# Performance work log

Measured on AMD Instinct MI355X. Metric: run time of the kernel, lower is better.

The kernel has to match this reference:

```python
import jax, jax.numpy as jnp
import numpy as np

B, T, D, F, E = 8, 2048, 1024, 4096, 16
C_FACTOR = 1.25
LB_W = 0.01


def setup_inputs() -> dict:
    key = jax.random.key(0)
    ks = jax.random.split(key, 4)
    x = jax.random.normal(ks[0], (B, T, D), dtype=jnp.float32)
    Wr = jax.random.normal(ks[1], (E, D), dtype=jnp.float32) * 0.02
    W1 = jax.random.normal(ks[2], (E, F, D), dtype=jnp.float32) * 0.02
    b1 = jnp.zeros((E, F), dtype=jnp.float32)
    W2 = jax.random.normal(ks[3], (E, D, F), dtype=jnp.float32) * 0.02
    b2 = jnp.zeros((E, D), dtype=jnp.float32)
    return {"x": x, "Wr": Wr, "W1": W1, "b1": b1, "W2": W2, "b2": b2}


def reference(x, Wr, W1, b1, W2, b2):
    Bs, Ts, Ds = x.shape
    Es = Wr.shape[0]
    tokens = Bs * Ts
    xf = x.reshape(tokens, Ds)

    # router
    logits = xf @ Wr.T                       # [tokens, E]
    probs = jax.nn.softmax(logits, axis=-1)
    top1 = jnp.argmax(probs, axis=-1)        # [tokens]
    top1p = jnp.max(probs, axis=-1)          # [tokens]

    capacity = int(C_FACTOR * tokens / Es)   # static python int

    onehot = jax.nn.one_hot(top1, Es, dtype=jnp.int32)        # [tokens, E]
    f = onehot.sum(axis=0).astype(probs.dtype) / tokens
    p = probs.mean(axis=0)
    lb_loss = Es * jnp.sum(f * p) * LB_W

    # faithful reproduction of idx[::expert_capacity]: among tokens routed to
    # expert e (in token order), keep only those whose rank % capacity == 0
    ranks = jnp.cumsum(onehot, axis=0) - 1                     # [tokens, E]
    keep = (onehot == 1) & (ranks % capacity == 0)             # [tokens, E]
    K = (tokens - 1) // capacity + 1                           # static max kept per expert

    idx = jax.vmap(lambda m: jnp.nonzero(m, size=K, fill_value=0)[0])(keep.T)  # [E, K]
    valid = jnp.take_along_axis(keep.T, idx, axis=1)           # [E, K] bool

    xg = xf[idx]                                               # [E, K, D]
    h = jax.nn.gelu(jnp.einsum('ekd,efd->ekf', xg, W1) + b1[:, None, :], approximate=False)
    eo = jnp.einsum('ekf,edf->ekd', h, W2) + b2[:, None, :]    # [E, K, D]
    scale = top1p[idx] * valid.astype(eo.dtype)                # [E, K]
    eo = eo * scale[..., None]

    out = jnp.zeros_like(xf).at[idx.reshape(-1)].add(eo.reshape(-1, Ds))
    return out.reshape(Bs, Ts, Ds), lb_loss
```

## Files before the change

### kernel.cpp

```cpp
#include <hip/hip_runtime.h>
#include <math.h>


#define TOKENS 16384
#define DD     1024
#define FF     4096
#define EE     16
#define CAP    1280
#define KMAX   13
#define NBLK   256

__global__ __launch_bounds__(256) void router_kernel(
    const float* __restrict__ x, const float* __restrict__ Wr,
    int* __restrict__ top1, float* __restrict__ top1p,
    int* __restrict__ blockhist, float* __restrict__ p_sums)
{
    __shared__ float wrj[EE * 256];
    __shared__ float p_acc[EE];
    __shared__ int   hist[EE];

    const int tid  = threadIdx.x;
    const int wave = tid >> 6;
    const int lane = tid & 63;
    const int blk  = blockIdx.x;

    if (tid < EE) { p_acc[tid] = 0.0f; hist[tid] = 0; }

    for (int it = 0; it < 4; ++it) {
        const int tbase = blk * 64 + wave * 16 + it * 4;

        float4 xr[4][4];
        #pragma unroll
        for (int t = 0; t < 4; ++t) {
            const float4* xp = (const float4*)(x + (size_t)(tbase + t) * DD);
            #pragma unroll
            for (int j = 0; j < 4; ++j) xr[t][j] = xp[j * 64 + lane];
        }

        float acc[4][EE];
        #pragma unroll
        for (int t = 0; t < 4; ++t)
            #pragma unroll
            for (int e = 0; e < EE; ++e) acc[t][e] = 0.0f;

        for (int j = 0; j < 4; ++j) {
            __syncthreads();
            #pragma unroll
            for (int k = 0; k < 4; ++k) {
                int i = tid + k * 256;
                int e = i >> 6, c = i & 63;
                ((float4*)wrj)[i] = ((const float4*)Wr)[e * 256 + j * 64 + c];
            }
            __syncthreads();
            #pragma unroll
            for (int e = 0; e < EE; ++e) {
                float4 w = ((const float4*)(wrj + e * 256))[lane];
                #pragma unroll
                for (int t = 0; t < 4; ++t) {
                    acc[t][e] += xr[t][j].x * w.x + xr[t][j].y * w.y
                               + xr[t][j].z * w.z + xr[t][j].w * w.w;
                }
            }
        }

        #pragma unroll
        for (int t = 0; t < 4; ++t)
            #pragma unroll
            for (int e = 0; e < EE; ++e) {
                float v = acc[t][e];
                v += __shfl_xor(v, 32);
                v += __shfl_xor(v, 16);
                v += __shfl_xor(v, 8);
                v += __shfl_xor(v, 4);
                v += __shfl_xor(v, 2);
                v += __shfl_xor(v, 1);
                acc[t][e] = v;
            }

        if (lane < 4) {
            float lg[EE];
            #pragma unroll
            for (int e = 0; e < EE; ++e) {
                float v = acc[3][e];
                if (lane == 2) v = acc[2][e];
                if (lane == 1) v = acc[1][e];
                if (lane == 0) v = acc[0][e];
                lg[e] = v;
            }
            const int gt = tbase + lane;
            float mx = lg[0]; int bi = 0;
            #pragma unroll
            for (int e = 1; e < EE; ++e)
                if (lg[e] > mx) { mx = lg[e]; bi = e; }
            float pr[EE];
            float s = 0.0f;
            #pragma unroll
            for (int e = 0; e < EE; ++e) { pr[e] = expf(lg[e] - mx); s += pr[e]; }
            const float inv = 1.0f / s;
            top1[gt]  = bi;
            top1p[gt] = inv;
            #pragma unroll
            for (int e = 0; e < EE; ++e) atomicAdd(&p_acc[e], pr[e] * inv);
            atomicAdd(&hist[bi], 1);
        }
    }
    __syncthreads();
    if (tid < EE) {
        blockhist[blk * EE + tid] = hist[tid];
        atomicAdd(&p_sums[tid], p_acc[tid]);
    }
}

__global__ __launch_bounds__(256) void scan_kernel(
    const int* __restrict__ blockhist, int* __restrict__ base,
    int* __restrict__ counts, int* __restrict__ nkept,
    const float* __restrict__ p_sums, const int* __restrict__ top1,
    float* __restrict__ mult0, float* __restrict__ lb_out)
{
    __shared__ int   hist_l[NBLK * EE];
    __shared__ int   gsum[EE * 16];
    __shared__ float fp[EE];
    __shared__ int   nk_l[EE];

    const int tid = threadIdx.x;
    for (int i = tid; i < NBLK * EE; i += 256) hist_l[i] = blockhist[i];
    __syncthreads();

    const int e = tid >> 4, g = tid & 15;
    int s = 0;
    for (int b = g * 16; b < g * 16 + 16; ++b) s += hist_l[b * EE + e];
    gsum[e * 16 + g] = s;
    __syncthreads();

    int pre = 0;
    for (int g2 = 0; g2 < g; ++g2) pre += gsum[e * 16 + g2];
    int run = pre;
    for (int b = g * 16; b < g * 16 + 16; ++b) {
        base[b * EE + e] = run;
        run += hist_l[b * EE + e];
    }
    if (g == 15) {
        const int c = run;
        counts[e] = c;
        const int nk = (c > 0) ? ((c - 1) / CAP + 1) : 0;
        nkept[e] = nk;
        nk_l[e]  = nk;
        fp[e] = ((float)c / (float)TOKENS) * (p_sums[e] / (float)TOKENS);
    }
    __syncthreads();
    if (tid == 0) {
        const int e0 = top1[0];
        mult0[0] = (float)(1 + KMAX - nk_l[e0]);
        float sum = 0.0f;
        for (int i = 0; i < EE; ++i) sum += fp[i];
        lb_out[0] = (float)EE * sum * 0.01f;
    }
}

__global__ __launch_bounds__(64) void keep_kernel(
    const int* __restrict__ top1, const float* __restrict__ top1p,
    const int* __restrict__ base, const float* __restrict__ mult0,
    int* __restrict__ kept_tok, float* __restrict__ kept_scale,
    int* __restrict__ slotmap)
{
    __shared__ int t1[64];
    const int tid = threadIdx.x;
    const int blk = blockIdx.x;
    const int gt  = blk * 64 + tid;
    const int e   = top1[gt];
    t1[tid] = e;
    __syncthreads();
    int r = 0;
    for (int i = 0; i < tid; ++i) r += (t1[i] == e) ? 1 : 0;
    const int rank = base[blk * EE + e] + r;
    if (rank % CAP == 0) {
        const int slot = rank / CAP;
        kept_tok[e * KMAX + slot] = gt;
        float sc = top1p[gt];
        if (gt == 0) sc *= mult0[0];
        kept_scale[e * KMAX + slot] = sc;
        slotmap[gt] = e * KMAX + slot;
    }
}

__global__ __launch_bounds__(256) void expert1_kernel(
    const float* __restrict__ x, const float* __restrict__ W1,
    const float* __restrict__ b1, const int* __restrict__ nkept,
    const int* __restrict__ kept_tok, float* __restrict__ h)
{
    const int e    = blockIdx.x >> 8;
    const int fblk = blockIdx.x & 255;
    const int ne   = nkept[e];
    if (ne == 0) return;
    const int wave = threadIdx.x >> 6;
    const int lane = threadIdx.x & 63;
    #pragma unroll
    for (int i = 0; i < 4; ++i) {
        const int f = fblk * 16 + wave * 4 + i;
        const float4* wrow = (const float4*)(W1 + ((size_t)e * FF + f) * DD);
        const float4 w0 = wrow[lane];
        const float4 w1 = wrow[64 + lane];
        const float4 w2 = wrow[128 + lane];
        const float4 w3 = wrow[192 + lane];
        for (int s = 0; s < ne; ++s) {
            const int t = kept_tok[e * KMAX + s];
            const float4* xp = (const float4*)(x + (size_t)t * DD);
            const float4 x0 = xp[lane];
            const float4 x1 = xp[64 + lane];
            const float4 x2 = xp[128 + lane];
            const float4 x3 = xp[192 + lane];
            float d = w0.x*x0.x + w0.y*x0.y + w0.z*x0.z + w0.w*x0.w
                    + w1.x*x1.x + w1.y*x1.y + w1.z*x1.z + w1.w*x1.w
                    + w2.x*x2.x + w2.y*x2.y + w2.z*x2.z + w2.w*x2.w
                    + w3.x*x3.x + w3.y*x3.y + w3.z*x3.z + w3.w*x3.w;
            d += __shfl_xor(d, 32);
            d += __shfl_xor(d, 16);
            d += __shfl_xor(d, 8);
            d += __shfl_xor(d, 4);
            d += __shfl_xor(d, 2);
            d += __shfl_xor(d, 1);
            if (lane == 0) {
                const float v = d + b1[e * FF + f];
                h[((size_t)e * KMAX + s) * FF + f] =
                    0.5f * v * (1.0f + erff(v * 0.70710678118654752440f));
            }
        }
    }
}

__global__ __launch_bounds__(256) void expert2_kernel(
    const float* __restrict__ h, const float* __restrict__ W2,
    const float* __restrict__ b2, const int* __restrict__ nkept,
    const float* __restrict__ kept_scale, float* __restrict__ eo)
{
    const int e    = blockIdx.x >> 6;
    const int dblk = blockIdx.x & 63;
    const int ne   = nkept[e];
    if (ne == 0) return;
    const int wave = threadIdx.x >> 6;
    const int lane = threadIdx.x & 63;
    #pragma unroll
    for (int i = 0; i < 4; ++i) {
        const int d = dblk * 16 + wave * 4 + i;
        const float4* wrow = (const float4*)(W2 + ((size_t)e * DD + d) * FF);
        float4 w[16];
        #pragma unroll
        for (int k = 0; k < 16; ++k) w[k] = wrow[k * 64 + lane];
        for (int s = 0; s < ne; ++s) {
            const float4* hp = (const float4*)(h + ((size_t)e * KMAX + s) * FF);
            float acc = 0.0f;
            #pragma unroll
            for (int k = 0; k < 16; ++k) {
                const float4 hv = hp[k * 64 + lane];
                acc += w[k].x*hv.x + w[k].y*hv.y + w[k].z*hv.z + w[k].w*hv.w;
            }
            acc += __shfl_xor(acc, 32);
            acc += __shfl_xor(acc, 16);
            acc += __shfl_xor(acc, 8);
            acc += __shfl_xor(acc, 4);
            acc += __shfl_xor(acc, 2);
            acc += __shfl_xor(acc, 1);
            if (lane == 0) {
                const float sc = kept_scale[e * KMAX + s];
                eo[((size_t)e * KMAX + s) * DD + d] = sc * (acc + b2[e * DD + d]);
            }
        }
    }
}

__global__ __launch_bounds__(256) void expand_kernel(
    const float* __restrict__ eo, const int* __restrict__ slotmap,
    float* __restrict__ out)
{
    const int nf4 = TOKENS * DD / 4;
    int idx = blockIdx.x * 256 + threadIdx.x;
    const int stride = 4096 * 256;
    for (; idx < nf4; idx += stride) {
        const int t    = idx >> 8;
        const int slot = slotmap[t];
        float4 v = make_float4(0.0f, 0.0f, 0.0f, 0.0f);
        if (slot >= 0) v = ((const float4*)eo)[slot * 256 + (idx & 255)];
        ((float4*)out)[idx] = v;
    }
}

extern "C" void kernel_launch(void* const* d_in, const int* in_sizes, int n_in,
                              void* d_out, int out_size, void* d_ws, size_t ws_size,
                              hipStream_t stream) {
    const float* x  = (const float*)d_in[0];
    const float* Wr = (const float*)d_in[1];
    const float* W1 = (const float*)d_in[2];
    const float* b1 = (const float*)d_in[3];
    const float* W2 = (const float*)d_in[4];
    const float* b2 = (const float*)d_in[5];
    float* out = (float*)d_out;

    char* p = (char*)d_ws;
    int*   top1       = (int*)p;    p += (size_t)TOKENS * 4;
    float* top1p      = (float*)p;  p += (size_t)TOKENS * 4;
    int*   slotmap    = (int*)p;    p += (size_t)TOKENS * 4;
    int*   blockhist  = (int*)p;    p += (size_t)NBLK * EE * 4;
    int*   base       = (int*)p;    p += (size_t)NBLK * EE * 4;
    int*   counts     = (int*)p;    p += (size_t)EE * 4;
    int*   nkept      = (int*)p;    p += (size_t)EE * 4;
    float* p_sums     = (float*)p;  p += (size_t)EE * 4;
    float* mult0      = (float*)p;  p += 16;
    int*   kept_tok   = (int*)p;    p += (size_t)EE * KMAX * 4;
    float* kept_scale = (float*)p;  p += (size_t)EE * KMAX * 4;
    float* eo         = (float*)p;  p += (size_t)EE * KMAX * DD * 4;
    float* h          = (float*)p;  p += (size_t)EE * KMAX * FF * 4;
    (void)ws_size; (void)in_sizes; (void)n_in; (void)counts;

    hipMemsetAsync(p_sums, 0, EE * sizeof(float), stream);
    hipMemsetAsync(slotmap, 0xFF, (size_t)TOKENS * sizeof(int), stream);

    router_kernel<<<NBLK, 256, 0, stream>>>(x, Wr, top1, top1p, blockhist, p_sums);
    scan_kernel<<<1, 256, 0, stream>>>(blockhist, base, counts, nkept, p_sums,
                                       top1, mult0, out + (size_t)out_size - 1);
    keep_kernel<<<NBLK, 64, 0, stream>>>(top1, top1p, base, mult0,
                                         kept_tok, kept_scale, slotmap);
    expert1_kernel<<<EE * 256, 256, 0, stream>>>(x, W1, b1, nkept, kept_tok, h);
    expert2_kernel<<<EE * 64, 256, 0, stream>>>(h, W2, b2, nkept, kept_scale, eo);
    expand_kernel<<<4096, 256, 0, stream>>>(eo, slotmap, out);
}
```

Before: 674.6 us.

## Fuse expert FFN GEMVs with F-chunked split-K and atomic accumulation

Merges the two expert kernels into one. Each block computes a 128-wide chunk of the GELU hidden activations into shared memory, then multiplies that chunk by the matching W2 columns and atomically adds partial outputs into a zeroed accumulator. Scale and bias move into the expand kernel. The two memsets are removed: per-block prob sums replace the global atomics, and keep_kernel now writes the full slotmap and zeroes the accumulator. This drops the global h round-trip and two launches, but the W2 reads become narrow float2 strided rows, and many float atomics add contention and make the summation order nondeterministic.

```diff
diff --git a/kernel.cpp b/kernel.cpp
--- a/kernel.cpp
+++ b/kernel.cpp
@@ -9,11 +9,13 @@
 #define CAP    1280
 #define KMAX   13
 #define NBLK   256
+#define FCH    128
+#define NCH    (FF / FCH)
 
 __global__ __launch_bounds__(256) void router_kernel(
     const float* __restrict__ x, const float* __restrict__ Wr,
     int* __restrict__ top1, float* __restrict__ top1p,
-    int* __restrict__ blockhist, float* __restrict__ p_sums)
+    int* __restrict__ blockhist, float* __restrict__ blockpsum)
 {
     __shared__ float wrj[EE * 256];
     __shared__ float p_acc[EE];
@@ -107,18 +109,19 @@
     __syncthreads();
     if (tid < EE) {
         blockhist[blk * EE + tid] = hist[tid];
-        atomicAdd(&p_sums[tid], p_acc[tid]);
+        blockpsum[blk * EE + tid] = p_acc[tid];
     }
 }
 
 __global__ __launch_bounds__(256) void scan_kernel(
-    const int* __restrict__ blockhist, int* __restrict__ base,
-    int* __restrict__ counts, int* __restrict__ nkept,
-    const float* __restrict__ p_sums, const int* __restrict__ top1,
-    float* __restrict__ mult0, float* __restrict__ lb_out)
+    const int* __restrict__ blockhist, const float* __restrict__ blockpsum,
+    int* __restrict__ base, int* __restrict__ nkept,
+    const int* __restrict__ top1, float* __restrict__ mult0,
+    float* __restrict__ lb_out)
 {
     __shared__ int   hist_l[NBLK * EE];
     __shared__ int   gsum[EE * 16];
+    __shared__ float fps[EE * 16];
     __shared__ float fp[EE];
     __shared__ int   nk_l[EE];
 
@@ -128,8 +131,13 @@
 
     const int e = tid >> 4, g = tid & 15;
     int s = 0;
-    for (int b = g * 16; b < g * 16 + 16; ++b) s += hist_l[b * EE + e];
+    float sp = 0.0f;
+    for (int b = g * 16; b < g * 16 + 16; ++b) {
+        s  += hist_l[b * EE + e];
+        sp += blockpsum[b * EE + e];
+    }
     gsum[e * 16 + g] = s;
+    fps[e * 16 + g]  = sp;
     __syncthreads();
 
     int pre = 0;
@@ -141,11 +149,12 @@
     }
     if (g == 15) {
         const int c = run;
-        counts[e] = c;
         const int nk = (c > 0) ? ((c - 1) / CAP + 1) : 0;
         nkept[e] = nk;
         nk_l[e]  = nk;
-        fp[e] = ((float)c / (float)TOKENS) * (p_sums[e] / (float)TOKENS);
+        float ps = 0.0f;
+        for (int g2 = 0; g2 < 16; ++g2) ps += fps[e * 16 + g2];
+        fp[e] = ((float)c / (float)TOKENS) * (ps / (float)TOKENS);
     }
     __syncthreads();
     if (tid == 0) {
@@ -161,7 +170,7 @@
     const int* __restrict__ top1, const float* __restrict__ top1p,
     const int* __restrict__ base, const float* __restrict__ mult0,
     int* __restrict__ kept_tok, float* __restrict__ kept_scale,
-    int* __restrict__ slotmap)
+    int* __restrict__ slotmap, float* __restrict__ acc)
 {
     __shared__ int t1[64];
     const int tid = threadIdx.x;
@@ -173,30 +182,42 @@
     int r = 0;
     for (int i = 0; i < tid; ++i) r += (t1[i] == e) ? 1 : 0;
     const int rank = base[blk * EE + e] + r;
+    int sm = -1;
     if (rank % CAP == 0) {
         const int slot = rank / CAP;
-        kept_tok[e * KMAX + slot] = gt;
+        sm = e * KMAX + slot;
+        kept_tok[sm] = gt;
         float sc = top1p[gt];
         if (gt == 0) sc *= mult0[0];
-        kept_scale[e * KMAX + slot] = sc;
-        slotmap[gt] = e * KMAX + slot;
-    }
-}
-
-__global__ __launch_bounds__(256) void expert1_kernel(
+        kept_scale[sm] = sc;
+    }
+    slotmap[gt] = sm;
+    float4* a4 = (float4*)acc;
+    for (int i = gt; i < EE * KMAX * DD / 4; i += NBLK * 64)
+        a4[i] = make_float4(0.0f, 0.0f, 0.0f, 0.0f);
+}
+
+__global__ __launch_bounds__(256) void expert_fused_kernel(
     const float* __restrict__ x, const float* __restrict__ W1,
-    const float* __restrict__ b1, const int* __restrict__ nkept,
-    const int* __restrict__ kept_tok, float* __restrict__ h)
-{
-    const int e    = blockIdx.x >> 8;
-    const int fblk = blockIdx.x & 255;
-    const int ne   = nkept[e];
+    const float* __restrict__ b1, const float* __restrict__ W2,
+    const int* __restrict__ nkept, const int* __restrict__ kept_tok,
+    float* __restrict__ acc)
+{
+    const int blk = blockIdx.x;
+    const int e   = blk >> 5;
+    const int ch  = blk & (NCH - 1);
+    const int f0  = ch * FCH;
+    const int ne  = nkept[e];
     if (ne == 0) return;
+
+    __shared__ float h_l[KMAX * FCH];
+
     const int wave = threadIdx.x >> 6;
     const int lane = threadIdx.x & 63;
-    #pragma unroll
-    for (int i = 0; i < 4; ++i) {
-        const int f = fblk * 16 + wave * 4 + i;
+
+    for (int r = 0; r < 32; ++r) {
+        const int cf = wave * 32 + r;
+        const int f  = f0 + cf;
         const float4* wrow = (const float4*)(W1 + ((size_t)e * FF + f) * DD);
         const float4 w0 = wrow[lane];
         const float4 w1 = wrow[64 + lane];
@@ -221,55 +242,34 @@
             d += __shfl_xor(d, 1);
             if (lane == 0) {
                 const float v = d + b1[e * FF + f];
-                h[((size_t)e * KMAX + s) * FF + f] =
+                h_l[s * FCH + cf] =
                     0.5f * v * (1.0f + erff(v * 0.70710678118654752440f));
             }
         }
     }
-}
-
-__global__ __launch_bounds__(256) void expert2_kernel(
-    const float* __restrict__ h, const float* __restrict__ W2,
-    const float* __restrict__ b2, const int* __restrict__ nkept,
-    const float* __restrict__ kept_scale, float* __restrict__ eo)
-{
-    const int e    = blockIdx.x >> 6;
-    const int dblk = blockIdx.x & 63;
-    const int ne   = nkept[e];
-    if (ne == 0) return;
-    const int wave = threadIdx.x >> 6;
-    const int lane = threadIdx.x & 63;
-    #pragma unroll
-    for (int i = 0; i < 4; ++i) {
-        const int d = dblk * 16 + wave * 4 + i;
-        const float4* wrow = (const float4*)(W2 + ((size_t)e * DD + d) * FF);
-        float4 w[16];
-        #pragma unroll
-        for (int k = 0; k < 16; ++k) w[k] = wrow[k * 64 + lane];
+    __syncthreads();
+
+    for (int i = 0; i < 256; ++i) {
+        const int d = wave * 256 + i;
+        const float2 w = ((const float2*)(W2 + ((size_t)e * DD + d) * FF + f0))[lane];
         for (int s = 0; s < ne; ++s) {
-            const float4* hp = (const float4*)(h + ((size_t)e * KMAX + s) * FF);
-            float acc = 0.0f;
-            #pragma unroll
-            for (int k = 0; k < 16; ++k) {
-                const float4 hv = hp[k * 64 + lane];
-                acc += w[k].x*hv.x + w[k].y*hv.y + w[k].z*hv.z + w[k].w*hv.w;
-            }
-            acc += __shfl_xor(acc, 32);
-            acc += __shfl_xor(acc, 16);
-            acc += __shfl_xor(acc, 8);
-            acc += __shfl_xor(acc, 4);
-            acc += __shfl_xor(acc, 2);
-            acc += __shfl_xor(acc, 1);
-            if (lane == 0) {
-                const float sc = kept_scale[e * KMAX + s];
-                eo[((size_t)e * KMAX + s) * DD + d] = sc * (acc + b2[e * DD + d]);
-            }
+            const float2 hv = ((const float2*)(h_l + s * FCH))[lane];
+            float v = w.x * hv.x + w.y * hv.y;
+            v += __shfl_xor(v, 32);
+            v += __shfl_xor(v, 16);
+            v += __shfl_xor(v, 8);
+            v += __shfl_xor(v, 4);
+            v += __shfl_xor(v, 2);
+            v += __shfl_xor(v, 1);
+            if (lane == 0)
+                atomicAdd(&acc[((size_t)e * KMAX + s) * DD + d], v);
         }
     }
 }
 
 __global__ __launch_bounds__(256) void expand_kernel(
-    const float* __restrict__ eo, const int* __restrict__ slotmap,
+    const float* __restrict__ acc, const float* __restrict__ kept_scale,
+    const float* __restrict__ b2, const int* __restrict__ slotmap,
     float* __restrict__ out)
 {
     const int nf4 = TOKENS * DD / 4;
@@ -279,7 +279,14 @@
         const int t    = idx >> 8;
         const int slot = slotmap[t];
         float4 v = make_float4(0.0f, 0.0f, 0.0f, 0.0f);
-        if (slot >= 0) v = ((const float4*)eo)[slot * 256 + (idx & 255)];
+        if (slot >= 0) {
+            const int e = slot / KMAX;
+            const float sc = kept_scale[slot];
+            const float4 a  = ((const float4*)acc)[slot * 256 + (idx & 255)];
+            const float4 bb = ((const float4*)b2)[e * 256 + (idx & 255)];
+            v = make_float4(sc * (a.x + bb.x), sc * (a.y + bb.y),
+                            sc * (a.z + bb.z), sc * (a.w + bb.w));
+        }
         ((float4*)out)[idx] = v;
     }
 }
@@ -300,26 +307,22 @@
     float* top1p      = (float*)p;  p += (size_t)TOKENS * 4;
     int*   slotmap    = (int*)p;    p += (size_t)TOKENS * 4;
     int*   blockhist  = (int*)p;    p += (size_t)NBLK * EE * 4;
+    float* blockpsum  = (float*)p;  p += (size_t)NBLK * EE * 4;
     int*   base       = (int*)p;    p += (size_t)NBLK * EE * 4;
-    int*   counts     = (int*)p;    p += (size_t)EE * 4;
-    int*   nkept      = (int*)p;    p += (size_t)EE * 4;
-    float* p_sums     = (float*)p;  p += (size_t)EE * 4;
-    float* mult0      = (float*)p;  p += 16;
-    int*   kept_tok   = (int*)p;    p += (size_t)EE * KMAX * 4;
-    float* kept_scale = (float*)p;  p += (size_t)EE * KMAX * 4;
-    float* eo         = (float*)p;  p += (size_t)EE * KMAX * DD * 4;
-    float* h          = (float*)p;  p += (size_t)EE * KMAX * FF * 4;
-    (void)ws_size; (void)in_sizes; (void)n_in; (void)counts;
-
-    hipMemsetAsync(p_sums, 0, EE * sizeof(float), stream);
-    hipMemsetAsync(slotmap, 0xFF, (size_t)TOKENS * sizeof(int), stream);
-
-    router_kernel<<<NBLK, 256, 0, stream>>>(x, Wr, top1, top1p, blockhist, p_sums);
-    scan_kernel<<<1, 256, 0, stream>>>(blockhist, base, counts, nkept, p_sums,
+    int*   nkept      = (int*)p;    p += 256;
+    float* mult0      = (float*)p;  p += 256;
+    int*   kept_tok   = (int*)p;    p += 1024;
+    float* kept_scale = (float*)p;  p += 1024;
+    float* acc        = (float*)p;  p += (size_t)EE * KMAX * DD * 4;
+    (void)ws_size; (void)in_sizes; (void)n_in;
+
+    router_kernel<<<NBLK, 256, 0, stream>>>(x, Wr, top1, top1p,
+                                            blockhist, blockpsum);
+    scan_kernel<<<1, 256, 0, stream>>>(blockhist, blockpsum, base, nkept,
                                        top1, mult0, out + (size_t)out_size - 1);
     keep_kernel<<<NBLK, 64, 0, stream>>>(top1, top1p, base, mult0,
-                                         kept_tok, kept_scale, slotmap);
-    expert1_kernel<<<EE * 256, 256, 0, stream>>>(x, W1, b1, nkept, kept_tok, h);
-    expert2_kernel<<<EE * 64, 256, 0, stream>>>(h, W2, b2, nkept, kept_scale, eo);
-    expand_kernel<<<4096, 256, 0, stream>>>(eo, slotmap, out);
-}
+                                         kept_tok, kept_scale, slotmap, acc);
+    expert_fused_kernel<<<EE * NCH, 256, 0, stream>>>(x, W1, b1, W2,
+                                                      nkept, kept_tok, acc);
+    expand_kernel<<<4096, 256, 0, stream>>>(acc, kept_scale, b2, slotmap, out);
+}
```

Measured after the change: 791.3 us. +17.3%, slower.

## Drop memsets, write per-block prob sums, stage h in LDS, reorder expert loops

Applied to the files above, without the earlier changes.

The router now writes per-block probability sums that the scan kernel reduces, and keep_kernel writes every slotmap entry. Together these remove both hipMemsetAsync calls and the global atomics. expert1 swaps its loops so each x row is loaded once per token and W1 rows are reread inside. expert2 stages each h row in shared memory and streams W2 from memory instead of holding 16 float4 weights in registers. This lowers register pressure and launch overhead, at the cost of rereading weight rows for every kept token (they probably hit in cache).

```diff
diff --git a/kernel.cpp b/kernel.cpp
--- a/kernel.cpp
+++ b/kernel.cpp
@@ -13,7 +13,7 @@
 __global__ __launch_bounds__(256) void router_kernel(
     const float* __restrict__ x, const float* __restrict__ Wr,
     int* __restrict__ top1, float* __restrict__ top1p,
-    int* __restrict__ blockhist, float* __restrict__ p_sums)
+    int* __restrict__ blockhist, float* __restrict__ blockpsum)
 {
     __shared__ float wrj[EE * 256];
     __shared__ float p_acc[EE];
@@ -107,18 +107,19 @@
     __syncthreads();
     if (tid < EE) {
         blockhist[blk * EE + tid] = hist[tid];
-        atomicAdd(&p_sums[tid], p_acc[tid]);
+        blockpsum[blk * EE + tid] = p_acc[tid];
     }
 }
 
 __global__ __launch_bounds__(256) void scan_kernel(
-    const int* __restrict__ blockhist, int* __restrict__ base,
-    int* __restrict__ counts, int* __restrict__ nkept,
-    const float* __restrict__ p_sums, const int* __restrict__ top1,
-    float* __restrict__ mult0, float* __restrict__ lb_out)
+    const int* __restrict__ blockhist, const float* __restrict__ blockpsum,
+    int* __restrict__ base, int* __restrict__ nkept,
+    const int* __restrict__ top1, float* __restrict__ mult0,
+    float* __restrict__ lb_out)
 {
     __shared__ int   hist_l[NBLK * EE];
     __shared__ int   gsum[EE * 16];
+    __shared__ float fps[EE * 16];
     __shared__ float fp[EE];
     __shared__ int   nk_l[EE];
 
@@ -128,8 +129,13 @@
 
     const int e = tid >> 4, g = tid & 15;
     int s = 0;
-    for (int b = g * 16; b < g * 16 + 16; ++b) s += hist_l[b * EE + e];
+    float sp = 0.0f;
+    for (int b = g * 16; b < g * 16 + 16; ++b) {
+        s  += hist_l[b * EE + e];
+        sp += blockpsum[b * EE + e];
+    }
     gsum[e * 16 + g] = s;
+    fps[e * 16 + g]  = sp;
     __syncthreads();
 
     int pre = 0;
@@ -141,11 +147,12 @@
     }
     if (g == 15) {
         const int c = run;
-        counts[e] = c;
         const int nk = (c > 0) ? ((c - 1) / CAP + 1) : 0;
         nkept[e] = nk;
         nk_l[e]  = nk;
-        fp[e] = ((float)c / (float)TOKENS) * (p_sums[e] / (float)TOKENS);
+        float ps = 0.0f;
+        for (int g2 = 0; g2 < 16; ++g2) ps += fps[e * 16 + g2];
+        fp[e] = ((float)c / (float)TOKENS) * (ps / (float)TOKENS);
     }
     __syncthreads();
     if (tid == 0) {
@@ -173,14 +180,16 @@
     int r = 0;
     for (int i = 0; i < tid; ++i) r += (t1[i] == e) ? 1 : 0;
     const int rank = base[blk * EE + e] + r;
+    int sm = -1;
     if (rank % CAP == 0) {
         const int slot = rank / CAP;
-        kept_tok[e * KMAX + slot] = gt;
+        sm = e * KMAX + slot;
+        kept_tok[sm] = gt;
         float sc = top1p[gt];
         if (gt == 0) sc *= mult0[0];
-        kept_scale[e * KMAX + slot] = sc;
-        slotmap[gt] = e * KMAX + slot;
-    }
+        kept_scale[sm] = sc;
+    }
+    slotmap[gt] = sm;
 }
 
 __global__ __launch_bounds__(256) void expert1_kernel(
@@ -194,21 +203,22 @@
     if (ne == 0) return;
     const int wave = threadIdx.x >> 6;
     const int lane = threadIdx.x & 63;
-    #pragma unroll
-    for (int i = 0; i < 4; ++i) {
-        const int f = fblk * 16 + wave * 4 + i;
-        const float4* wrow = (const float4*)(W1 + ((size_t)e * FF + f) * DD);
-        const float4 w0 = wrow[lane];
-        const float4 w1 = wrow[64 + lane];
-        const float4 w2 = wrow[128 + lane];
-        const float4 w3 = wrow[192 + lane];
-        for (int s = 0; s < ne; ++s) {
-            const int t = kept_tok[e * KMAX + s];
-            const float4* xp = (const float4*)(x + (size_t)t * DD);
-            const float4 x0 = xp[lane];
-            const float4 x1 = xp[64 + lane];
-            const float4 x2 = xp[128 + lane];
-            const float4 x3 = xp[192 + lane];
+
+    for (int s = 0; s < ne; ++s) {
+        const int t = kept_tok[e * KMAX + s];
+        const float4* xp = (const float4*)(x + (size_t)t * DD);
+        const float4 x0 = xp[lane];
+        const float4 x1 = xp[64 + lane];
+        const float4 x2 = xp[128 + lane];
+        const float4 x3 = xp[192 + lane];
+        #pragma unroll
+        for (int i = 0; i < 4; ++i) {
+            const int f = fblk * 16 + wave * 4 + i;
+            const float4* wrow = (const float4*)(W1 + ((size_t)e * FF + f) * DD);
+            const float4 w0 = wrow[lane];
+            const float4 w1 = wrow[64 + lane];
+            const float4 w2 = wrow[128 + lane];
+            const float4 w3 = wrow[192 + lane];
             float d = w0.x*x0.x + w0.y*x0.y + w0.z*x0.z + w0.w*x0.w
                     + w1.x*x1.x + w1.y*x1.y + w1.z*x1.z + w1.w*x1.w
                     + w2.x*x2.x + w2.y*x2.y + w2.z*x2.z + w2.w*x2.w
@@ -239,20 +249,29 @@
     if (ne == 0) return;
     const int wave = threadIdx.x >> 6;
     const int lane = threadIdx.x & 63;
-    #pragma unroll
-    for (int i = 0; i < 4; ++i) {
-        const int d = dblk * 16 + wave * 4 + i;
-        const float4* wrow = (const float4*)(W2 + ((size_t)e * DD + d) * FF);
-        float4 w[16];
-        #pragma unroll
-        for (int k = 0; k < 16; ++k) w[k] = wrow[k * 64 + lane];
-        for (int s = 0; s < ne; ++s) {
-            const float4* hp = (const float4*)(h + ((size_t)e * KMAX + s) * FF);
+    const int tid  = threadIdx.x;
+
+    __shared__ float hs[FF];
+
+    for (int s = 0; s < ne; ++s) {
+        if (s > 0) __syncthreads();
+        const float4* hp = (const float4*)(h + ((size_t)e * KMAX + s) * FF);
+        #pragma unroll
+        for (int k = 0; k < 4; ++k)
+            ((float4*)hs)[tid + k * 256] = hp[tid + k * 256];
+        __syncthreads();
+
+        const float sc = kept_scale[e * KMAX + s];
+        #pragma unroll
+        for (int i = 0; i < 4; ++i) {
+            const int d = dblk * 16 + wave * 4 + i;
+            const float4* wrow = (const float4*)(W2 + ((size_t)e * DD + d) * FF);
             float acc = 0.0f;
             #pragma unroll
             for (int k = 0; k < 16; ++k) {
-                const float4 hv = hp[k * 64 + lane];
-                acc += w[k].x*hv.x + w[k].y*hv.y + w[k].z*hv.z + w[k].w*hv.w;
+                const float4 w  = wrow[k * 64 + lane];
+                const float4 hv = ((const float4*)hs)[k * 64 + lane];
+                acc += w.x*hv.x + w.y*hv.y + w.z*hv.z + w.w*hv.w;
             }
             acc += __shfl_xor(acc, 32);
             acc += __shfl_xor(acc, 16);
@@ -260,10 +279,8 @@
             acc += __shfl_xor(acc, 4);
             acc += __shfl_xor(acc, 2);
             acc += __shfl_xor(acc, 1);
-            if (lane == 0) {
-                const float sc = kept_scale[e * KMAX + s];
+            if (lane == 0)
                 eo[((size_t)e * KMAX + s) * DD + d] = sc * (acc + b2[e * DD + d]);
-            }
         }
     }
 }
@@ -300,22 +317,19 @@
     float* top1p      = (float*)p;  p += (size_t)TOKENS * 4;
     int*   slotmap    = (int*)p;    p += (size_t)TOKENS * 4;
     int*   blockhist  = (int*)p;    p += (size_t)NBLK * EE * 4;
+    float* blockpsum  = (float*)p;  p += (size_t)NBLK * EE * 4;
     int*   base       = (int*)p;    p += (size_t)NBLK * EE * 4;
-    int*   counts     = (int*)p;    p += (size_t)EE * 4;
-    int*   nkept      = (int*)p;    p += (size_t)EE * 4;
-    float* p_sums     = (float*)p;  p += (size_t)EE * 4;
-    float* mult0      = (float*)p;  p += 16;
-    int*   kept_tok   = (int*)p;    p += (size_t)EE * KMAX * 4;
-    float* kept_scale = (float*)p;  p += (size_t)EE * KMAX * 4;
+    int*   nkept      = (int*)p;    p += 256;
+    float* mult0      = (float*)p;  p += 256;
+    int*   kept_tok   = (int*)p;    p += 1024;
+    float* kept_scale = (float*)p;  p += 1024;
     float* eo         = (float*)p;  p += (size_t)EE * KMAX * DD * 4;
     float* h          = (float*)p;  p += (size_t)EE * KMAX * FF * 4;
-    (void)ws_size; (void)in_sizes; (void)n_in; (void)counts;
-
-    hipMemsetAsync(p_sums, 0, EE * sizeof(float), stream);
-    hipMemsetAsync(slotmap, 0xFF, (size_t)TOKENS * sizeof(int), stream);
-
-    router_kernel<<<NBLK, 256, 0, stream>>>(x, Wr, top1, top1p, blockhist, p_sums);
-    scan_kernel<<<1, 256, 0, stream>>>(blockhist, base, counts, nkept, p_sums,
+    (void)ws_size; (void)in_sizes; (void)n_in;
+
+    router_kernel<<<NBLK, 256, 0, stream>>>(x, Wr, top1, top1p,
+                                            blockhist, blockpsum);
+    scan_kernel<<<1, 256, 0, stream>>>(blockhist, blockpsum, base, nkept,
                                        top1, mult0, out + (size_t)out_size - 1);
     keep_kernel<<<NBLK, 64, 0, stream>>>(top1, top1p, base, mult0,
                                          kept_tok, kept_scale, slotmap);
```

Result: no change. 674.8 us (+0.0%).
